# Kernel tuning notes

Hardware: AMD Instinct MI355X
Metric: run time of the kernel (lower is better)

Reference implementation:

```python
import jax, jax.numpy as jnp
import numpy as np

B, C, H, W = 4, 64, 256, 256
HEADS = 4
HID = 128  # dim * ffn_expansion_factor
EPS = 1e-5


def _ln_chan(x, w, b):
    # LayerNorm over channel axis of [b,c,h,w] (equiv to to_3d -> LN over c -> to_4d)
    mu = x.mean(1, keepdims=True)
    var = jnp.mean((x - mu) ** 2, axis=1, keepdims=True)
    return (x - mu) / jnp.sqrt(var + EPS) * w[None, :, None, None] + b[None, :, None, None]


def _ln_last(x, w, b):
    mu = x.mean(-1, keepdims=True)
    var = jnp.mean((x - mu) ** 2, axis=-1, keepdims=True)
    return (x - mu) / jnp.sqrt(var + EPS) * w + b


def _conv1(x, Wt):
    # 1x1 conv, no bias; Wt: [out,in]
    return jnp.einsum('oi,bihw->bohw', Wt, x)


def _l2norm(x):
    # torch F.normalize(dim=-1): x / max(||x||, 1e-12)
    return x / jnp.maximum(jnp.linalg.norm(x, axis=-1, keepdims=True), 1e-12)


def _dct(inp1, inp2, Wq, Wk, Wv, temp):
    # Divide_Cross_Transformer: q from inp2, k/v from inp1; channel-wise attention
    b, c, h, w = inp1.shape
    ch = c // HEADS
    hw = h * w
    q = _conv1(inp2, Wq).reshape(b, HEADS, ch, hw)
    k = _conv1(inp1, Wk).reshape(b, HEADS, ch, hw)
    v = _conv1(inp1, Wv).reshape(b, HEADS, ch, hw)
    q = _l2norm(q)
    k = _l2norm(k)
    attn = jax.nn.softmax(jnp.einsum('bhcn,bhdn->bhcd', q, k) * temp[None], axis=-1)
    return attn, v  # attn: [b,head,ch,ch], v: [b,head,ch,hw]


def _ffn(x3, w1, b1, w2, b2):
    # torch nn.GELU default = exact erf
    hdn = jax.nn.gelu(jnp.einsum('bnc,hc->bnh', x3, w1) + b1, approximate=False)
    return jnp.einsum('bnh,ch->bnc', hdn, w2) + b2


def setup_inputs() -> dict:
    key = jax.random.key(0)
    ks = jax.random.split(key, 16)
    s = 0.05

    def n(k, shape):
        return jax.random.normal(k, shape, jnp.float32) * s

    ones = jnp.ones((C,), jnp.float32)
    zeros = jnp.zeros((C,), jnp.float32)
    return {
        'image': jax.random.normal(ks[0], (B, C, H, W), jnp.float32),
        'event': jax.random.normal(ks[1], (B, C, H, W), jnp.float32),
        'Wq_c': n(ks[2], (C, C)), 'Wk_c': n(ks[3], (C, C)), 'Wv_c': n(ks[4], (C, C)),
        'temp_c': jnp.ones((HEADS, 1, 1), jnp.float32),
        'Wq_d': n(ks[5], (C, C)), 'Wk_d': n(ks[6], (C, C)), 'Wv_d': n(ks[7], (C, C)),
        'temp_d': jnp.ones((HEADS, 1, 1), jnp.float32),
        'ln_img_w': ones, 'ln_img_b': zeros,
        'ln_evt_w': ones, 'ln_evt_b': zeros,
        'ln_com_w': ones, 'ln_com_b': zeros,
        'ln_dif_w': ones, 'ln_dif_b': zeros,
        'ln1_w': ones, 'ln1_b': zeros,
        'ln2_w': ones, 'ln2_b': zeros,
        'fc1c_w': n(ks[8], (HID, C)), 'fc1c_b': jnp.zeros((HID,), jnp.float32),
        'fc2c_w': n(ks[9], (C, HID)), 'fc2c_b': jnp.zeros((C,), jnp.float32),
        'fc1d_w': n(ks[10], (HID, C)), 'fc1d_b': jnp.zeros((HID,), jnp.float32),
        'fc2d_w': n(ks[11], (C, HID)), 'fc2d_b': jnp.zeros((C,), jnp.float32),
        'proj1_w': n(ks[12], (C, C)), 'proj2_w': n(ks[13], (C, C)),
    }


def reference(image, event, Wq_c, Wk_c, Wv_c, temp_c, Wq_d, Wk_d, Wv_d, temp_d,
              ln_img_w, ln_img_b, ln_evt_w, ln_evt_b, ln_com_w, ln_com_b,
              ln_dif_w, ln_dif_b, ln1_w, ln1_b, ln2_w, ln2_b,
              fc1c_w, fc1c_b, fc2c_w, fc2c_b, fc1d_w, fc1d_b, fc2d_w, fc2d_b,
              proj1_w, proj2_w):
    b, c, h, w = image.shape
    hw = h * w
    common = image + event
    differential = image - event

    ni = _ln_chan(image, ln_img_w, ln_img_b)
    ne = _ln_chan(event, ln_evt_w, ln_evt_b)
    nc = _ln_chan(common, ln_com_w, ln_com_b)
    nd = _ln_chan(differential, ln_dif_w, ln_dif_b)

    # common branch: shared conv weights (attn_common), attn maps multiplied
    a_ic, v_ic = _dct(ni, nc, Wq_c, Wk_c, Wv_c, temp_c)
    a_ec, v_ec = _dct(ne, nc, Wq_c, Wk_c, Wv_c, temp_c)
    a_c = a_ic * a_ec
    oc = jnp.einsum('bhcd,bhdn->bhcn', a_c, v_ic + v_ec)  # same attn for both matmuls
    oc = oc.reshape(b, c, h, w)
    oc = _conv1(oc, proj1_w)
    oc3 = oc.reshape(b, c, hw).transpose(0, 2, 1)  # b (hw) c
    oc3 = oc3 + _ffn(_ln_last(oc3, ln1_w, ln1_b), fc1c_w, fc1c_b, fc2c_w, fc2c_b)
    out_common = oc3.transpose(0, 2, 1).reshape(b, c, h, w)

    # differential branch: separate attn maps, not multiplied
    a_id, v_id = _dct(ni, nd, Wq_d, Wk_d, Wv_d, temp_d)
    a_ed, v_ed = _dct(ne, nd, Wq_d, Wk_d, Wv_d, temp_d)
    od = (jnp.einsum('bhcd,bhdn->bhcn', a_id, v_id)
          + jnp.einsum('bhcd,bhdn->bhcn', a_ed, v_ed))
    od = od.reshape(b, c, h, w)
    od = _conv1(od, proj2_w)
    od3 = od.reshape(b, c, hw).transpose(0, 2, 1)
    od3 = od3 + _ffn(_ln_last(od3, ln2_w, ln2_b), fc1d_w, fc1d_b, fc2d_w, fc2d_b)
    out_differential = od3.transpose(0, 2, 1).reshape(b, c, h, w)

    return (out_common, out_differential)
```

## Files before the change

### kernel.cpp

```cpp
#include <hip/hip_runtime.h>
#include <math.h>

typedef unsigned int u32;
typedef unsigned short u16;
typedef __attribute__((ext_vector_type(8))) short short8;
typedef __attribute__((ext_vector_type(4))) float float4v;

#define NBATCH 4
#define HW 65536

#define OFF_COV 0
#define OFF_T   131072
#define OFF_M   294912
#define OFF_P   344064
#define OFF_WC  393216
#define OFF_PAR 516096
#define WS_NEED ((size_t)(OFF_PAR + 1048576) * 4)

__device__ inline float bf2f(u16 h){ return __uint_as_float(((u32)h) << 16); }
__device__ inline u16 f2bf(float x){
  u32 u = __float_as_uint(x);
  u += 0x7fffu + ((u >> 16) & 1u);
  return (u16)(u >> 16);
}
__device__ inline u32 packbf2(float a, float b){
  return (u32)f2bf(a) | ((u32)f2bf(b) << 16);
}
__device__ inline float bfu(u32 u, int hi){
  return __uint_as_float(hi ? (u & 0xffff0000u) : (u << 16));
}

__device__ inline bool detect_f32(const void* probe, int t, int* s_cnt){
  if (t == 0) *s_cnt = 0;
  __syncthreads();
  u32 w = ((const u32*)probe)[t & 255];
  u32 ex = (w >> 7) & 0xffu;
  if (!(ex >= 113u && ex <= 133u)) atomicAdd(s_cnt, 1);
  __syncthreads();
  return *s_cnt >= 128;
}

__device__ inline void ld8(const u16* pb, const float* pf, size_t idx, bool f32, float* o){
  if (f32){
    const float4 a = *(const float4*)(pf + idx);
    const float4 b = *(const float4*)(pf + idx + 4);
    o[0]=a.x; o[1]=a.y; o[2]=a.z; o[3]=a.w; o[4]=b.x; o[5]=b.y; o[6]=b.z; o[7]=b.w;
  } else {
    uint4 r = *(const uint4*)(pb + idx);
    const u32* p = (const u32*)&r;
    #pragma unroll
    for (int j=0;j<8;j++) o[j] = bfu(p[j>>1], j&1);
  }
}

__device__ inline void softmax16(float* l){
  float m = l[0];
  #pragma unroll
  for (int i=1;i<16;i++) m = fmaxf(m, l[i]);
  float s = 0.f;
  #pragma unroll
  for (int i=0;i<16;i++){ l[i] = __expf(l[i]-m); s += l[i]; }
  float r = 1.0f/s;
  #pragma unroll
  for (int i=0;i<16;i++) l[i] *= r;
}

__global__ __launch_bounds__(256) void convert_all(
    const void* img,
    const void* t0, const void* t1, const void* t2, const void* t3,
    const void* t4, const void* t5, const void* t6, const void* t7,
    const void* t8, const void* t9, const void* t10, const void* t11,
    const void* t12, const void* t13, const void* t14, const void* t15,
    const void* t16, const void* t17, const void* t18, const void* t19,
    const void* t20, const void* t21, const void* t22, const void* t23,
    const void* t24, const void* t25, const void* t26, const void* t27,
    const void* t28, const void* t29,
    u16* __restrict__ wc)
{
  __shared__ int s_cnt;
  const int t = threadIdx.x;
  const bool f32 = detect_f32(img, t, &s_cnt);
  const int sizes[30] = {4096,4096,4096,4,4096,4096,4096,4,
                         64,64,64,64,64,64,64,64,64,64,64,64,
                         8192,128,8192,64,8192,128,8192,64,4096,4096};
  const void* srcs[30] = {t0,t1,t2,t3,t4,t5,t6,t7,t8,t9,t10,t11,t12,t13,t14,
                          t15,t16,t17,t18,t19,t20,t21,t22,t23,t24,t25,t26,t27,t28,t29};
  const int id = blockIdx.x;
  const void* s = srcs[id];
  const int n = sizes[id];
  u16* d = wc + (size_t)id*8192;
  for (int j = t; j < n; j += 256)
    d[j] = f32 ? f2bf(((const float*)s)[j]) : ((const u16*)s)[j];
}

__global__ __launch_bounds__(256) void k1_cov(
    const void* __restrict__ img, const void* __restrict__ evt,
    const u16* __restrict__ lniw, const u16* __restrict__ lnib,
    const u16* __restrict__ lnew, const u16* __restrict__ lneb,
    const u16* __restrict__ lncw, const u16* __restrict__ lncb,
    const u16* __restrict__ lndw, const u16* __restrict__ lndb,
    float* __restrict__ cov, float* __restrict__ par, int use_par)
{
  __shared__ u16 NtL[4*64*72];
  __shared__ float spart[4][64][5];
  __shared__ float params[64][8];
  __shared__ int s_cnt;

  const int t = threadIdx.x;
  const bool f32 = detect_f32(img, t, &s_cnt);
  const u16* imgb = (const u16*)img; const float* imgf = (const float*)img;
  const u16* evtb = (const u16*)evt; const float* evtf = (const float*)evt;

  const int b = blockIdx.x >> 7;
  const int P0 = (blockIdx.x & 127) * 512;
  const int chg = t >> 3, pg = t & 7, ch0 = chg*2;
  const int wave = t >> 6, lane = t & 63, l15 = lane & 15, quad = lane >> 4;

  float wi0=bf2f(lniw[ch0]), wi1=bf2f(lniw[ch0+1]);
  float bi0=bf2f(lnib[ch0]), bi1=bf2f(lnib[ch0+1]);
  float we0=bf2f(lnew[ch0]), we1=bf2f(lnew[ch0+1]);
  float be0=bf2f(lneb[ch0]), be1=bf2f(lneb[ch0+1]);
  float wc0=bf2f(lncw[ch0]), wc1=bf2f(lncw[ch0+1]);
  float bc0=bf2f(lncb[ch0]), bc1=bf2f(lncb[ch0+1]);
  float wd0=bf2f(lndw[ch0]), wd1=bf2f(lndw[ch0+1]);
  float bd0=bf2f(lndb[ch0]), bd1=bf2f(lndb[ch0+1]);

  int va1, vb1, va2, vb2;
  if (wave == 0){ va1=2; vb1=2; va2=2; vb2=0; }
  else if (wave == 1){ va1=2; vb1=1; va2=0; vb2=0; }
  else if (wave == 2){ va1=3; vb1=3; va2=3; vb2=0; }
  else { va1=3; vb1=1; va2=1; vb2=1; }

  float4v acc0[4][4], acc1v[4][4];
  #pragma unroll
  for (int i=0;i<4;i++)
    #pragma unroll
    for (int j=0;j<4;j++){ acc0[i][j]=(float4v)0.f; acc1v[i][j]=(float4v)0.f; }

  const size_t base_i = (size_t)(b*64 + ch0) * HW;

  for (int it = 0; it < 8; ++it){
    const int p0 = P0 + it*64;
    float A0[8], A1[8], B0[8], B1[8];
    ld8(imgb, imgf, base_i + p0 + pg*8, f32, A0);
    ld8(imgb, imgf, base_i + HW + p0 + pg*8, f32, A1);
    ld8(evtb, evtf, base_i + p0 + pg*8, f32, B0);
    ld8(evtb, evtf, base_i + HW + p0 + pg*8, f32, B1);

    float si[8], sii[8], se[8], see[8], sie[8];
    #pragma unroll
    for (int j=0;j<8;j++){
      float xi0=A0[j], xi1=A1[j], xe0=B0[j], xe1=B1[j];
      si[j]  = xi0 + xi1;
      sii[j] = fmaf(xi0, xi0, xi1*xi1);
      se[j]  = xe0 + xe1;
      see[j] = fmaf(xe0, xe0, xe1*xe1);
      sie[j] = fmaf(xi0, xe0, xi1*xe1);
    }
    #pragma unroll
    for (int m=8; m<=32; m<<=1){
      #pragma unroll
      for (int j=0;j<8;j++){
        si[j]  += __shfl_xor(si[j],  m);
        sii[j] += __shfl_xor(sii[j], m);
        se[j]  += __shfl_xor(se[j],  m);
        see[j] += __shfl_xor(see[j], m);
        sie[j] += __shfl_xor(sie[j], m);
      }
    }
    if ((chg & 7) == 0){
      #pragma unroll
      for (int j=0;j<8;j++){
        spart[wave][pg*8+j][0]=si[j];  spart[wave][pg*8+j][1]=sii[j];
        spart[wave][pg*8+j][2]=se[j];  spart[wave][pg*8+j][3]=see[j];
        spart[wave][pg*8+j][4]=sie[j];
      }
    }
    __syncthreads();
    if (t < 64){
      float S0=0,S1=0,S2=0,S3=0,S4=0;
      #pragma unroll
      for (int w=0;w<4;w++){
        S0+=spart[w][t][0]; S1+=spart[w][t][1]; S2+=spart[w][t][2];
        S3+=spart[w][t][3]; S4+=spart[w][t][4];
      }
      const float inv = 0.015625f;
      float mu_i=S0*inv, mu_e=S2*inv;
      float r_i = rsqrtf(fmaf(S1,inv,-mu_i*mu_i)+1e-5f);
      float r_e = rsqrtf(fmaf(S3,inv,-mu_e*mu_e)+1e-5f);
      float mu_c=mu_i+mu_e, mu_d=mu_i-mu_e;
      float r_c = rsqrtf((S1+2.f*S4+S3)*inv - mu_c*mu_c + 1e-5f);
      float r_d = rsqrtf((S1-2.f*S4+S3)*inv - mu_d*mu_d + 1e-5f);
      params[t][0]=mu_i; params[t][1]=r_i; params[t][2]=mu_e; params[t][3]=r_e;
      params[t][4]=mu_c; params[t][5]=r_c; params[t][6]=mu_d; params[t][7]=r_d;
      if (use_par){
        float4 pv; pv.x=mu_i; pv.y=r_i; pv.z=mu_e; pv.w=r_e;
        *(float4*)(par + ((size_t)b*HW + p0 + t)*4) = pv;
      }
    }
    __syncthreads();
    u32 un[4][2][4];
    #pragma unroll
    for (int jj=0;jj<4;jj++){
      float4 pA0 = *(const float4*)&params[pg*8+jj*2][0];
      float4 pB0 = *(const float4*)&params[pg*8+jj*2][4];
      float4 pA1 = *(const float4*)&params[pg*8+jj*2+1][0];
      float4 pB1 = *(const float4*)&params[pg*8+jj*2+1][4];
      float xiA0=A0[2*jj], xiA1=A1[2*jj], xeA0=B0[2*jj], xeA1=B1[2*jj];
      float xiB0=A0[2*jj+1], xiB1=A1[2*jj+1], xeB0=B0[2*jj+1], xeB1=B1[2*jj+1];
      un[0][0][jj] = packbf2(fmaf((xiA0-pA0.x)*pA0.y, wi0, bi0), fmaf((xiB0-pA1.x)*pA1.y, wi0, bi0));
      un[0][1][jj] = packbf2(fmaf((xiA1-pA0.x)*pA0.y, wi1, bi1), fmaf((xiB1-pA1.x)*pA1.y, wi1, bi1));
      un[1][0][jj] = packbf2(fmaf((xeA0-pA0.z)*pA0.w, we0, be0), fmaf((xeB0-pA1.z)*pA1.w, we0, be0));
      un[1][1][jj] = packbf2(fmaf((xeA1-pA0.z)*pA0.w, we1, be1), fmaf((xeB1-pA1.z)*pA1.w, we1, be1));
      float xcA0=xiA0+xeA0, xcA1=xiA1+xeA1, xcB0=xiB0+xeB0, xcB1=xiB1+xeB1;
      un[2][0][jj] = packbf2(fmaf((xcA0-pB0.x)*pB0.y, wc0, bc0), fmaf((xcB0-pB1.x)*pB1.y, wc0, bc0));
      un[2][1][jj] = packbf2(fmaf((xcA1-pB0.x)*pB0.y, wc1, bc1), fmaf((xcB1-pB1.x)*pB1.y, wc1, bc1));
      float xdA0=xiA0-xeA0, xdA1=xiA1-xeA1, xdB0=xiB0-xeB0, xdB1=xiB1-xeB1;
      un[3][0][jj] = packbf2(fmaf((xdA0-pB0.z)*pB0.w, wd0, bd0), fmaf((xdB0-pB1.z)*pB1.w, wd0, bd0));
      un[3][1][jj] = packbf2(fmaf((xdA1-pB0.z)*pB0.w, wd1, bd1), fmaf((xdB1-pB1.z)*pB1.w, wd1, bd1));
    }
    #pragma unroll
    for (int v=0; v<4; v++){
      *(uint4*)&NtL[(v*64 + ch0  )*72 + pg*8] = make_uint4(un[v][0][0],un[v][0][1],un[v][0][2],un[v][0][3]);
      *(uint4*)&NtL[(v*64 + ch0+1)*72 + pg*8] = make_uint4(un[v][1][0],un[v][1][1],un[v][1][2],un[v][1][3]);
    }
    __syncthreads();
    #pragma unroll
    for (int ks=0; ks<2; ks++){
      const int off = ks*32 + quad*8;
      short8 A1f[4], B1f[4], A2f[4], B2f[4];
      #pragma unroll
      for (int mi=0;mi<4;mi++){
        A1f[mi] = *(const short8*)&NtL[(va1*64 + mi*16 + l15)*72 + off];
        B1f[mi] = *(const short8*)&NtL[(vb1*64 + mi*16 + l15)*72 + off];
        A2f[mi] = *(const short8*)&NtL[(va2*64 + mi*16 + l15)*72 + off];
        B2f[mi] = *(const short8*)&NtL[(vb2*64 + mi*16 + l15)*72 + off];
      }
      #pragma unroll
      for (int mi=0;mi<4;mi++)
        #pragma unroll
        for (int nj=0;nj<4;nj++){
          acc0[mi][nj]  = __builtin_amdgcn_mfma_f32_16x16x32_bf16(A1f[mi], B1f[nj], acc0[mi][nj], 0,0,0);
          acc1v[mi][nj] = __builtin_amdgcn_mfma_f32_16x16x32_bf16(A2f[mi], B2f[nj], acc1v[mi][nj], 0,0,0);
        }
    }
  }
  float* c0 = cov + ((size_t)(wave*2 + 0)*NBATCH + b)*4096;
  float* c1 = cov + ((size_t)(wave*2 + 1)*NBATCH + b)*4096;
  #pragma unroll
  for (int mi=0;mi<4;mi++)
    #pragma unroll
    for (int nj=0;nj<4;nj++){
      int row0 = mi*16 + quad*4, col = nj*16 + l15;
      #pragma unroll
      for (int r=0;r<4;r++){
        atomicAdd(&c0[(row0+r)*64 + col], acc0[mi][nj][r]);
        atomicAdd(&c1[(row0+r)*64 + col], acc1v[mi][nj][r]);
      }
    }
}

__global__ __launch_bounds__(256) void p2a(
    const u16* __restrict__ Wq_c, const u16* __restrict__ Wk_c,
    const u16* __restrict__ Wq_d, const u16* __restrict__ Wk_d,
    float* __restrict__ ws)
{
  __shared__ float WL[64][65];
  __shared__ float CL[64][64];
  const int t = threadIdx.x;
  const int b = blockIdx.x & 3;
  const int which = blockIdx.x >> 2;
  int wsel, csel;
  switch (which){
    case 0: wsel=0; csel=0; break;
    case 1: wsel=1; csel=3; break;
    case 2: wsel=1; csel=7; break;
    case 3: wsel=2; csel=4; break;
    case 4: wsel=3; csel=3; break;
    case 5: wsel=3; csel=7; break;
    case 6: wsel=0; csel=1; break;
    case 7: wsel=0; csel=2; break;
    case 8: wsel=2; csel=5; break;
    default: wsel=2; csel=6; break;
  }
  const u16* W = (wsel==0)? Wq_c : (wsel==1)? Wk_c : (wsel==2)? Wq_d : Wk_d;
  const float* Cm = ws + ((size_t)csel*NBATCH + b)*4096;
  { int r = t>>2, c0 = (t&3)*16;
    #pragma unroll
    for (int i=0;i<16;i++) WL[r][c0+i] = bf2f(W[r*64 + c0 + i]);
    const float4* s = (const float4*)(Cm + r*64 + c0);
    float4* d = (float4*)&CL[r][c0];
    d[0]=s[0]; d[1]=s[1]; d[2]=s[2]; d[3]=s[3]; }
  __syncthreads();
  const int r = t>>2, k0 = (t&3)*16;
  float a[16];
  #pragma unroll
  for (int i=0;i<16;i++) a[i]=0.f;
  for (int m=0;m<64;m++){
    float wv = WL[r][m];
    #pragma unroll
    for (int i=0;i<16;i++) a[i] = fmaf(wv, CL[m][k0+i], a[i]);
  }
  float* o = ws + OFF_T + ((size_t)which*NBATCH + b)*4096 + r*64 + k0;
  #pragma unroll
  for (int i=0;i<16;i++) o[i] = a[i];
}

__global__ __launch_bounds__(256) void p2b(
    float* __restrict__ ws,
    const u16* __restrict__ Wq_c, const u16* __restrict__ Wk_c,
    const u16* __restrict__ Wq_d, const u16* __restrict__ Wk_d,
    const u16* __restrict__ Wv_c, const u16* __restrict__ Wv_d,
    const u16* __restrict__ temp_c, const u16* __restrict__ temp_d)
{
  const int b = blockIdx.x, t = threadIdx.x;
  __shared__ float rn[6][64];
  __shared__ float GLs[4][64][16];
  __shared__ float AL[3][64][16];
  const float* T = ws + OFF_T;
  {
    int s = t>>6, c = t&63;
    const float* Tp = T + ((size_t)s*NBATCH + b)*4096 + c*64;
    const u16* Wp = (s==0)? Wq_c : (s==3)? Wq_d : Wk_c;
    float acc=0;
    for (int k=0;k<64;k++) acc = fmaf(Tp[k], bf2f(Wp[c*64+k]), acc);
    rn[s][c] = 1.0f/fmaxf(sqrtf(fmaxf(acc,0.f)), 1e-12f);
    if (t < 128){
      int s2 = 4 + (t>>6);
      const float* Tp2 = T + ((size_t)s2*NBATCH + b)*4096 + c*64;
      float acc2=0;
      for (int k=0;k<64;k++) acc2 = fmaf(Tp2[k], bf2f(Wk_d[c*64+k]), acc2);
      rn[s2][c] = 1.0f/fmaxf(sqrtf(fmaxf(acc2,0.f)), 1e-12f);
    }
  }
  #pragma unroll 1
  for (int i=0;i<16;i++){
    int e = t*16 + i;
    int s = e >> 10, c = (e>>4)&63, dl = e&15, d = (c&~15)+dl;
    const float* Tp = T + ((size_t)(6+s)*NBATCH + b)*4096 + c*64;
    const u16* Wp = ((s<2)? Wk_c : Wk_d) + d*64;
    float acc=0;
    for (int j=0;j<64;j++) acc = fmaf(Tp[j], bf2f(Wp[j]), acc);
    GLs[s][c][dl] = acc;
  }
  __syncthreads();
  if (t < 192){
    int set = t>>6, c = t&63, h = c>>4, cb = c&~15;
    if (set == 0){
      float tc = bf2f(temp_c[h]);
      float rq = rn[0][c];
      float l1[16], l2[16];
      #pragma unroll
      for (int dl=0;dl<16;dl++){
        l1[dl] = GLs[0][c][dl]*rq*rn[1][cb+dl]*tc;
        l2[dl] = GLs[1][c][dl]*rq*rn[2][cb+dl]*tc;
      }
      softmax16(l1); softmax16(l2);
      #pragma unroll
      for (int dl=0;dl<16;dl++) AL[0][c][dl] = l1[dl]*l2[dl];
    } else {
      float td = bf2f(temp_d[h]);
      float rq = rn[3][c];
      int gi = (set==1)? 2 : 3;
      int rk = (set==1)? 4 : 5;
      float l[16];
      #pragma unroll
      for (int dl=0;dl<16;dl++) l[dl] = GLs[gi][c][dl]*rq*rn[rk][cb+dl]*td;
      softmax16(l);
      #pragma unroll
      for (int dl=0;dl<16;dl++) AL[set][c][dl] = l[dl];
    }
  }
  __syncthreads();
  for (int wsel=0; wsel<3; wsel++){
    const u16* Wv = (wsel==0)? Wv_c : Wv_d;
    #pragma unroll 1
    for (int i=0;i<16;i++){
      int e = t*16+i, c = e>>6, k = e&63, cb = c&~15;
      float acc=0;
      #pragma unroll
      for (int dl=0;dl<16;dl++) acc = fmaf(AL[wsel][c][dl], bf2f(Wv[(cb+dl)*64 + k]), acc);
      ws[OFF_M + ((size_t)wsel*NBATCH + b)*4096 + c*64 + k] = acc;
    }
  }
}

__global__ __launch_bounds__(256) void p2c(
    const u16* __restrict__ proj1, const u16* __restrict__ proj2,
    float* __restrict__ ws)
{
  __shared__ float WL[64][65];
  __shared__ float CL[64][64];
  const int t = threadIdx.x;
  const int b = blockIdx.x & 3;
  const int which = blockIdx.x >> 2;
  const u16* W = (which==0)? proj1 : proj2;
  const float* Cm = ws + OFF_M + ((size_t)which*NBATCH + b)*4096;
  { int r = t>>2, c0 = (t&3)*16;
    #pragma unroll
    for (int i=0;i<16;i++) WL[r][c0+i] = bf2f(W[r*64 + c0 + i]);
    const float4* s = (const float4*)(Cm + r*64 + c0);
    float4* d = (float4*)&CL[r][c0];
    d[0]=s[0]; d[1]=s[1]; d[2]=s[2]; d[3]=s[3]; }
  __syncthreads();
  const int r = t>>2, k0 = (t&3)*16;
  float a[16];
  #pragma unroll
  for (int i=0;i<16;i++) a[i]=0.f;
  for (int m=0;m<64;m++){
    float wv = WL[r][m];
    #pragma unroll
    for (int i=0;i<16;i++) a[i] = fmaf(wv, CL[m][k0+i], a[i]);
  }
  float* o = ws + OFF_P + ((size_t)which*NBATCH + b)*4096 + r*64 + k0;
  #pragma unroll
  for (int i=0;i<16;i++) o[i] = a[i];
}

__global__ __launch_bounds__(256) void k3_common(
    const void* __restrict__ img, const void* __restrict__ evt,
    const u16* __restrict__ lniw, const u16* __restrict__ lnib,
    const u16* __restrict__ lnew, const u16* __restrict__ lneb,
    const u16* __restrict__ ln1w, const u16* __restrict__ ln1b,
    const u16* __restrict__ fc1w, const u16* __restrict__ fc1b,
    const u16* __restrict__ fc2w, const u16* __restrict__ fc2b,
    const float* __restrict__ Pmat, void* __restrict__ outp, size_t obase,
    const float* __restrict__ par, int use_par)
{
  __shared__ u16 fc1L[128*72];
  __shared__ u16 fc2L[64*136];
  __shared__ u16 PcL[64*72];
  __shared__ u16 SB[64*136];
  __shared__ float spart[4][64][4];
  __shared__ float params[64][4];
  __shared__ float b1L[128];
  __shared__ float b2L[64];
  __shared__ int s_cnt;

  const int t = threadIdx.x;
  const bool f32 = detect_f32(img, t, &s_cnt);
  const u16* imgb = (const u16*)img; const float* imgf = (const float*)img;
  const u16* evtb = (const u16*)evt; const float* evtf = (const float*)evt;

  const int b = blockIdx.x >> 8;
  const int P0 = (blockIdx.x & 255) * 256;
  const int chg = t >> 3, pg = t & 7, ch0 = chg*2;
  const int wave = t >> 6, lane = t & 63, l15 = lane & 15, quad = lane >> 4;

  { int row = t >> 1, c0 = (t & 1)*32;
    const uint4* s = (const uint4*)(fc1w + row*64 + c0);
    uint4* d = (uint4*)&fc1L[row*72 + c0];
    d[0]=s[0]; d[1]=s[1]; d[2]=s[2]; d[3]=s[3]; }
  { int row = t >> 2, c0 = (t & 3)*32;
    const uint4* s = (const uint4*)(fc2w + row*128 + c0);
    uint4* d = (uint4*)&fc2L[row*136 + c0];
    d[0]=s[0]; d[1]=s[1]; d[2]=s[2]; d[3]=s[3]; }
  { int row = t >> 2, c0 = (t & 3)*16;
    const float* s = Pmat + (size_t)b*4096 + row*64 + c0;
    u32 u[8];
    #pragma unroll
    for (int i=0;i<8;i++) u[i] = packbf2(s[2*i], s[2*i+1]);
    uint4* d = (uint4*)&PcL[row*72 + c0];
    d[0] = make_uint4(u[0],u[1],u[2],u[3]);
    d[1] = make_uint4(u[4],u[5],u[6],u[7]); }
  if (t < 128) b1L[t] = bf2f(fc1b[t]);
  if (t < 64)  b2L[t] = bf2f(fc2b[t]);

  float wi0=bf2f(lniw[ch0]), wi1=bf2f(lniw[ch0+1]);
  float we0=bf2f(lnew[ch0]), we1=bf2f(lnew[ch0+1]);
  float bs0=bf2f(lnib[ch0]) + bf2f(lneb[ch0]);
  float bs1=bf2f(lnib[ch0+1]) + bf2f(lneb[ch0+1]);
  float w1r[4], b1r[4];
  #pragma unroll
  for (int nj=0;nj<4;nj++){ w1r[nj]=bf2f(ln1w[nj*16+l15]); b1r[nj]=bf2f(ln1b[nj*16+l15]); }
  __syncthreads();

  const size_t base_i = (size_t)(b*64 + ch0)*HW;
  for (int it=0; it<4; ++it){
    const int p0 = P0 + it*64;
    float A0[8], A1[8], B0[8], B1[8];
    ld8(imgb, imgf, base_i + p0 + pg*8, f32, A0);
    ld8(imgb, imgf, base_i + HW + p0 + pg*8, f32, A1);
    ld8(evtb, evtf, base_i + p0 + pg*8, f32, B0);
    ld8(evtb, evtf, base_i + HW + p0 + pg*8, f32, B1);

    if (use_par){
      const float4* pp = (const float4*)(par + ((size_t)b*HW + p0 + pg*8)*4);
      #pragma unroll
      for (int j=0;j<8;j++){
        float4 pr = pp[j];
        float a0=(A0[j]-pr.x)*pr.y, a1=(A1[j]-pr.x)*pr.y;
        float c0f=(B0[j]-pr.z)*pr.w, c1f=(B1[j]-pr.z)*pr.w;
        float n0 = fmaf(a0, wi0, fmaf(c0f, we0, bs0));
        float n1 = fmaf(a1, wi1, fmaf(c1f, we1, bs1));
        *(u32*)&SB[(pg*8+j)*136 + ch0] = packbf2(n0, n1);
      }
    } else {
      float si[8], sii[8], se[8], see[8];
      #pragma unroll
      for (int j=0;j<8;j++){
        float xi0=A0[j], xi1=A1[j], xe0=B0[j], xe1=B1[j];
        si[j]=xi0+xi1; sii[j]=fmaf(xi0,xi0,xi1*xi1);
        se[j]=xe0+xe1; see[j]=fmaf(xe0,xe0,xe1*xe1);
      }
      #pragma unroll
      for (int m=8;m<=32;m<<=1)
        #pragma unroll
        for (int j=0;j<8;j++){
          si[j]+=__shfl_xor(si[j],m); sii[j]+=__shfl_xor(sii[j],m);
          se[j]+=__shfl_xor(se[j],m); see[j]+=__shfl_xor(see[j],m);
        }
      if ((chg&7)==0){
        #pragma unroll
        for (int j=0;j<8;j++){
          spart[wave][pg*8+j][0]=si[j]; spart[wave][pg*8+j][1]=sii[j];
          spart[wave][pg*8+j][2]=se[j]; spart[wave][pg*8+j][3]=see[j];
        }
      }
      __syncthreads();
      if (t<64){
        float S0=0,S1=0,S2=0,S3=0;
        #pragma unroll
        for (int w=0;w<4;w++){ S0+=spart[w][t][0]; S1+=spart[w][t][1]; S2+=spart[w][t][2]; S3+=spart[w][t][3]; }
        const float inv=0.015625f;
        float mu_i=S0*inv, mu_e=S2*inv;
        float r_i=rsqrtf(fmaf(S1,inv,-mu_i*mu_i)+1e-5f);
        float r_e=rsqrtf(fmaf(S3,inv,-mu_e*mu_e)+1e-5f);
        params[t][0]=mu_i; params[t][1]=r_i; params[t][2]=mu_e; params[t][3]=r_e;
      }
      __syncthreads();
      #pragma unroll
      for (int j=0;j<8;j++){
        float4 pr = *(const float4*)&params[pg*8+j][0];
        float a0=(A0[j]-pr.x)*pr.y, a1=(A1[j]-pr.x)*pr.y;
        float c0f=(B0[j]-pr.z)*pr.w, c1f=(B1[j]-pr.z)*pr.w;
        float n0 = fmaf(a0, wi0, fmaf(c0f, we0, bs0));
        float n1 = fmaf(a1, wi1, fmaf(c1f, we1, bs1));
        *(u32*)&SB[(pg*8+j)*136 + ch0] = packbf2(n0, n1);
      }
    }
    __syncthreads();
    float4v acc1[4];
    #pragma unroll
    for (int nj=0;nj<4;nj++) acc1[nj]=(float4v)0.f;
    const int px_row = wave*16 + l15;
    #pragma unroll
    for (int ks=0;ks<2;ks++){
      const int off = ks*32 + quad*8;
      short8 af = *(const short8*)&SB[px_row*136 + off];
      #pragma unroll
      for (int nj=0;nj<4;nj++){
        short8 bw = *(const short8*)&PcL[(nj*16+l15)*72 + off];
        acc1[nj] = __builtin_amdgcn_mfma_f32_16x16x32_bf16(af, bw, acc1[nj], 0,0,0);
      }
    }
    float s[4], sq[4];
    #pragma unroll
    for (int j=0;j<4;j++){
      s[j] = acc1[0][j]+acc1[1][j]+acc1[2][j]+acc1[3][j];
      sq[j] = acc1[0][j]*acc1[0][j];
      sq[j] = fmaf(acc1[1][j],acc1[1][j],sq[j]);
      sq[j] = fmaf(acc1[2][j],acc1[2][j],sq[j]);
      sq[j] = fmaf(acc1[3][j],acc1[3][j],sq[j]);
    }
    #pragma unroll
    for (int m=1;m<=8;m<<=1)
      #pragma unroll
      for (int j=0;j<4;j++){ s[j]+=__shfl_xor(s[j],m); sq[j]+=__shfl_xor(sq[j],m); }
    float muj[4], rj[4];
    #pragma unroll
    for (int j=0;j<4;j++){
      muj[j]=s[j]*0.015625f;
      rj[j]=rsqrtf(fmaf(sq[j],0.015625f,-muj[j]*muj[j])+1e-5f);
    }
    #pragma unroll
    for (int nj=0;nj<4;nj++)
      #pragma unroll
      for (int j=0;j<4;j++){
        float tv = (acc1[nj][j]-muj[j])*rj[j];
        tv = fmaf(tv, w1r[nj], b1r[nj]);
        SB[(wave*16+quad*4+j)*136 + nj*16+l15] = f2bf(tv);
      }
    float4v accF[8];
    #pragma unroll
    for (int nh=0;nh<8;nh++) accF[nh]=(float4v)0.f;
    #pragma unroll
    for (int ks=0;ks<2;ks++){
      const int off = ks*32+quad*8;
      short8 af = *(const short8*)&SB[px_row*136 + off];
      #pragma unroll
      for (int nh=0;nh<8;nh++){
        short8 bw = *(const short8*)&fc1L[(nh*16+l15)*72 + off];
        accF[nh] = __builtin_amdgcn_mfma_f32_16x16x32_bf16(af, bw, accF[nh], 0,0,0);
      }
    }
    #pragma unroll
    for (int nh=0;nh<8;nh++){
      float bb = b1L[nh*16+l15];
      #pragma unroll
      for (int j=0;j<4;j++){
        float v = accF[nh][j] + bb;
        float g = 0.5f*v*(1.0f + erff(v*0.70710678118654752f));
        SB[(wave*16+quad*4+j)*136 + nh*16+l15] = f2bf(g);
      }
    }
    float4v accO[4];
    #pragma unroll
    for (int nj=0;nj<4;nj++) accO[nj]=(float4v)0.f;
    #pragma unroll
    for (int ks=0;ks<4;ks++){
      const int off = ks*32+quad*8;
      short8 ag = *(const short8*)&SB[px_row*136 + off];
      #pragma unroll
      for (int nj=0;nj<4;nj++){
        short8 bw = *(const short8*)&fc2L[(nj*16+l15)*136 + off];
        accO[nj] = __builtin_amdgcn_mfma_f32_16x16x32_bf16(ag, bw, accO[nj], 0,0,0);
      }
    }
    const int px0 = p0 + wave*16 + quad*4;
    #pragma unroll
    for (int nj=0;nj<4;nj++){
      float bb = b2L[nj*16+l15];
      int r = nj*16+l15;
      float v0 = acc1[nj][0] + accO[nj][0] + bb;
      float v1 = acc1[nj][1] + accO[nj][1] + bb;
      float v2 = acc1[nj][2] + accO[nj][2] + bb;
      float v3 = acc1[nj][3] + accO[nj][3] + bb;
      size_t oi = obase + (size_t)(b*64 + r)*HW + px0;
      if (f32){ float4 fv; fv.x=v0; fv.y=v1; fv.z=v2; fv.w=v3;
        *(float4*)((float*)outp + oi) = fv; }
      else *(uint2*)((u16*)outp + oi) = make_uint2(packbf2(v0,v1), packbf2(v2,v3));
    }
    __syncthreads();
  }
}

__global__ __launch_bounds__(256) void k3_diff(
    const void* __restrict__ img, const void* __restrict__ evt,
    const u16* __restrict__ lniw, const u16* __restrict__ lnib,
    const u16* __restrict__ lnew, const u16* __restrict__ lneb,
    const u16* __restrict__ ln2w, const u16* __restrict__ ln2b,
    const u16* __restrict__ fc1w, const u16* __restrict__ fc1b,
    const u16* __restrict__ fc2w, const u16* __restrict__ fc2b,
    const float* __restrict__ Pmat, void* __restrict__ outp, size_t obase,
    const float* __restrict__ par, int use_par)
{
  __shared__ u16 fc1L[128*72];
  __shared__ u16 fc2L[64*136];
  __shared__ u16 PiL[64*72];
  __shared__ u16 PeL[64*72];
  __shared__ u16 N2L[64*144];
  __shared__ float spart[4][64][4];
  __shared__ float params[64][4];
  __shared__ float b1L[128];
  __shared__ float b2L[64];
  __shared__ int s_cnt;

  const int t = threadIdx.x;
  const bool f32 = detect_f32(img, t, &s_cnt);
  const u16* imgb = (const u16*)img; const float* imgf = (const float*)img;
  const u16* evtb = (const u16*)evt; const float* evtf = (const float*)evt;

  const int b = blockIdx.x >> 8;
  const int P0 = (blockIdx.x & 255) * 256;
  const int chg = t >> 3, pg = t & 7, ch0 = chg*2;
  const int wave = t >> 6, lane = t & 63, l15 = lane & 15, quad = lane >> 4;

  { int row = t >> 1, c0 = (t & 1)*32;
    const uint4* s = (const uint4*)(fc1w + row*64 + c0);
    uint4* d = (uint4*)&fc1L[row*72 + c0];
    d[0]=s[0]; d[1]=s[1]; d[2]=s[2]; d[3]=s[3]; }
  { int row = t >> 2, c0 = (t & 3)*32;
    const uint4* s = (const uint4*)(fc2w + row*128 + c0);
    uint4* d = (uint4*)&fc2L[row*136 + c0];
    d[0]=s[0]; d[1]=s[1]; d[2]=s[2]; d[3]=s[3]; }
  { int row = t >> 2, c0 = (t & 3)*16;
    const float* si_ = Pmat + ((size_t)1*NBATCH + b)*4096 + row*64 + c0;
    const float* se_ = Pmat + ((size_t)2*NBATCH + b)*4096 + row*64 + c0;
    u32 u[8];
    #pragma unroll
    for (int i=0;i<8;i++) u[i] = packbf2(si_[2*i], si_[2*i+1]);
    uint4* d = (uint4*)&PiL[row*72 + c0];
    d[0] = make_uint4(u[0],u[1],u[2],u[3]); d[1] = make_uint4(u[4],u[5],u[6],u[7]);
    #pragma unroll
    for (int i=0;i<8;i++) u[i] = packbf2(se_[2*i], se_[2*i+1]);
    uint4* d2 = (uint4*)&PeL[row*72 + c0];
    d2[0] = make_uint4(u[0],u[1],u[2],u[3]); d2[1] = make_uint4(u[4],u[5],u[6],u[7]); }
  if (t < 128) b1L[t] = bf2f(fc1b[t]);
  if (t < 64)  b2L[t] = bf2f(fc2b[t]);

  float wi0=bf2f(lniw[ch0]), wi1=bf2f(lniw[ch0+1]);
  float bi0=bf2f(lnib[ch0]), bi1=bf2f(lnib[ch0+1]);
  float we0=bf2f(lnew[ch0]), we1=bf2f(lnew[ch0+1]);
  float be0=bf2f(lneb[ch0]), be1=bf2f(lneb[ch0+1]);
  float w1r[4], b1r[4];
  #pragma unroll
  for (int nj=0;nj<4;nj++){ w1r[nj]=bf2f(ln2w[nj*16+l15]); b1r[nj]=bf2f(ln2b[nj*16+l15]); }
  __syncthreads();

  const size_t base_i = (size_t)(b*64 + ch0)*HW;
  for (int it=0; it<4; ++it){
    const int p0 = P0 + it*64;
    float A0[8], A1[8], B0[8], B1[8];
    ld8(imgb, imgf, base_i + p0 + pg*8, f32, A0);
    ld8(imgb, imgf, base_i + HW + p0 + pg*8, f32, A1);
    ld8(evtb, evtf, base_i + p0 + pg*8, f32, B0);
    ld8(evtb, evtf, base_i + HW + p0 + pg*8, f32, B1);

    if (use_par){
      const float4* pp = (const float4*)(par + ((size_t)b*HW + p0 + pg*8)*4);
      #pragma unroll
      for (int j=0;j<8;j++){
        float4 pr = pp[j];
        float a0=(A0[j]-pr.x)*pr.y, a1=(A1[j]-pr.x)*pr.y;
        float c0f=(B0[j]-pr.z)*pr.w, c1f=(B1[j]-pr.z)*pr.w;
        *(u32*)&N2L[(pg*8+j)*144 + ch0]      = packbf2(fmaf(a0,wi0,bi0), fmaf(a1,wi1,bi1));
        *(u32*)&N2L[(pg*8+j)*144 + 72 + ch0] = packbf2(fmaf(c0f,we0,be0), fmaf(c1f,we1,be1));
      }
    } else {
      float si[8], sii[8], se[8], see[8];
      #pragma unroll
      for (int j=0;j<8;j++){
        float xi0=A0[j], xi1=A1[j], xe0=B0[j], xe1=B1[j];
        si[j]=xi0+xi1; sii[j]=fmaf(xi0,xi0,xi1*xi1);
        se[j]=xe0+xe1; see[j]=fmaf(xe0,xe0,xe1*xe1);
      }
      #pragma unroll
      for (int m=8;m<=32;m<<=1)
        #pragma unroll
        for (int j=0;j<8;j++){
          si[j]+=__shfl_xor(si[j],m); sii[j]+=__shfl_xor(sii[j],m);
          se[j]+=__shfl_xor(se[j],m); see[j]+=__shfl_xor(see[j],m);
        }
      if ((chg&7)==0){
        #pragma unroll
        for (int j=0;j<8;j++){
          spart[wave][pg*8+j][0]=si[j]; spart[wave][pg*8+j][1]=sii[j];
          spart[wave][pg*8+j][2]=se[j]; spart[wave][pg*8+j][3]=see[j];
        }
      }
      __syncthreads();
      if (t<64){
        float S0=0,S1=0,S2=0,S3=0;
        #pragma unroll
        for (int w=0;w<4;w++){ S0+=spart[w][t][0]; S1+=spart[w][t][1]; S2+=spart[w][t][2]; S3+=spart[w][t][3]; }
        const float inv=0.015625f;
        float mu_i=S0*inv, mu_e=S2*inv;
        float r_i=rsqrtf(fmaf(S1,inv,-mu_i*mu_i)+1e-5f);
        float r_e=rsqrtf(fmaf(S3,inv,-mu_e*mu_e)+1e-5f);
        params[t][0]=mu_i; params[t][1]=r_i; params[t][2]=mu_e; params[t][3]=r_e;
      }
      __syncthreads();
      #pragma unroll
      for (int j=0;j<8;j++){
        float4 pr = *(const float4*)&params[pg*8+j][0];
        float a0=(A0[j]-pr.x)*pr.y, a1=(A1[j]-pr.x)*pr.y;
        float c0f=(B0[j]-pr.z)*pr.w, c1f=(B1[j]-pr.z)*pr.w;
        *(u32*)&N2L[(pg*8+j)*144 + ch0]      = packbf2(fmaf(a0,wi0,bi0), fmaf(a1,wi1,bi1));
        *(u32*)&N2L[(pg*8+j)*144 + 72 + ch0] = packbf2(fmaf(c0f,we0,be0), fmaf(c1f,we1,be1));
      }
    }
    __syncthreads();
    float4v acc1[4];
    #pragma unroll
    for (int nj=0;nj<4;nj++) acc1[nj]=(float4v)0.f;
    const int px_row = wave*16 + l15;
    #pragma unroll
    for (int ks=0;ks<2;ks++){
      const int off = ks*32 + quad*8;
      short8 ai = *(const short8*)&N2L[px_row*144 + off];
      short8 ae = *(const short8*)&N2L[px_row*144 + 72 + off];
      #pragma unroll
      for (int nj=0;nj<4;nj++){
        short8 bwi = *(const short8*)&PiL[(nj*16+l15)*72 + off];
        acc1[nj] = __builtin_amdgcn_mfma_f32_16x16x32_bf16(ai, bwi, acc1[nj], 0,0,0);
        short8 bwe = *(const short8*)&PeL[(nj*16+l15)*72 + off];
        acc1[nj] = __builtin_amdgcn_mfma_f32_16x16x32_bf16(ae, bwe, acc1[nj], 0,0,0);
      }
    }
    float s[4], sq[4];
    #pragma unroll
    for (int j=0;j<4;j++){
      s[j] = acc1[0][j]+acc1[1][j]+acc1[2][j]+acc1[3][j];
      sq[j] = acc1[0][j]*acc1[0][j];
      sq[j] = fmaf(acc1[1][j],acc1[1][j],sq[j]);
      sq[j] = fmaf(acc1[2][j],acc1[2][j],sq[j]);
      sq[j] = fmaf(acc1[3][j],acc1[3][j],sq[j]);
    }
    #pragma unroll
    for (int m=1;m<=8;m<<=1)
      #pragma unroll
      for (int j=0;j<4;j++){ s[j]+=__shfl_xor(s[j],m); sq[j]+=__shfl_xor(sq[j],m); }
    float muj[4], rj[4];
    #pragma unroll
    for (int j=0;j<4;j++){
      muj[j]=s[j]*0.015625f;
      rj[j]=rsqrtf(fmaf(sq[j],0.015625f,-muj[j]*muj[j])+1e-5f);
    }
    #pragma unroll
    for (int nj=0;nj<4;nj++)
      #pragma unroll
      for (int j=0;j<4;j++){
        float tv = (acc1[nj][j]-muj[j])*rj[j];
        tv = fmaf(tv, w1r[nj], b1r[nj]);
        N2L[(wave*16+quad*4+j)*144 + nj*16+l15] = f2bf(tv);
      }
    float4v accF[8];
    #pragma unroll
    for (int nh=0;nh<8;nh++) accF[nh]=(float4v)0.f;
    #pragma unroll
    for (int ks=0;ks<2;ks++){
      const int off = ks*32+quad*8;
      short8 af = *(const short8*)&N2L[px_row*144 + off];
      #pragma unroll
      for (int nh=0;nh<8;nh++){
        short8 bw = *(const short8*)&fc1L[(nh*16+l15)*72 + off];
        accF[nh] = __builtin_amdgcn_mfma_f32_16x16x32_bf16(af, bw, accF[nh], 0,0,0);
      }
    }
    #pragma unroll
    for (int nh=0;nh<8;nh++){
      float bb = b1L[nh*16+l15];
      #pragma unroll
      for (int j=0;j<4;j++){
        float v = accF[nh][j] + bb;
        float g = 0.5f*v*(1.0f + erff(v*0.70710678118654752f));
        N2L[(wave*16+quad*4+j)*144 + nh*16+l15] = f2bf(g);
      }
    }
    float4v accO[4];
    #pragma unroll
    for (int nj=0;nj<4;nj++) accO[nj]=(float4v)0.f;
    #pragma unroll
    for (int ks=0;ks<4;ks++){
      const int off = ks*32+quad*8;
      short8 ag = *(const short8*)&N2L[px_row*144 + off];
      #pragma unroll
      for (int nj=0;nj<4;nj++){
        short8 bw = *(const short8*)&fc2L[(nj*16+l15)*136 + off];
        accO[nj] = __builtin_amdgcn_mfma_f32_16x16x32_bf16(ag, bw, accO[nj], 0,0,0);
      }
    }
    const int px0 = p0 + wave*16 + quad*4;
    #pragma unroll
    for (int nj=0;nj<4;nj++){
      float bb = b2L[nj*16+l15];
      int r = nj*16+l15;
      float v0 = acc1[nj][0] + accO[nj][0] + bb;
      float v1 = acc1[nj][1] + accO[nj][1] + bb;
      float v2 = acc1[nj][2] + accO[nj][2] + bb;
      float v3 = acc1[nj][3] + accO[nj][3] + bb;
      size_t oi = obase + (size_t)(b*64 + r)*HW + px0;
      if (f32){ float4 fv; fv.x=v0; fv.y=v1; fv.z=v2; fv.w=v3;
        *(float4*)((float*)outp + oi) = fv; }
      else *(uint2*)((u16*)outp + oi) = make_uint2(packbf2(v0,v1), packbf2(v2,v3));
    }
    __syncthreads();
  }
}

extern "C" void kernel_launch(void* const* d_in, const int* in_sizes, int n_in,
                              void* d_out, int out_size, void* d_ws, size_t ws_size,
                              hipStream_t stream)
{
  const void* img = d_in[0];
  const void* evt = d_in[1];
  float* ws = (float*)d_ws;
  u16* wc = (u16*)(ws + OFF_WC);
  float* par = ws + OFF_PAR;
  const int use_par = (ws_size >= WS_NEED) ? 1 : 0;
  #define SLOT(i) (wc + (size_t)((i)-2)*8192)

  hipMemsetAsync(ws, 0, 131072*sizeof(float), stream);
  convert_all<<<dim3(30), dim3(256), 0, stream>>>(img,
      d_in[2], d_in[3], d_in[4], d_in[5], d_in[6], d_in[7], d_in[8], d_in[9],
      d_in[10], d_in[11], d_in[12], d_in[13], d_in[14], d_in[15], d_in[16], d_in[17],
      d_in[18], d_in[19], d_in[20], d_in[21], d_in[22], d_in[23], d_in[24], d_in[25],
      d_in[26], d_in[27], d_in[28], d_in[29], d_in[30], d_in[31], wc);
  k1_cov<<<dim3(512), dim3(256), 0, stream>>>(img, evt,
      SLOT(10), SLOT(11), SLOT(12), SLOT(13), SLOT(14), SLOT(15), SLOT(16), SLOT(17),
      ws, par, use_par);
  p2a<<<dim3(40), dim3(256), 0, stream>>>(SLOT(2), SLOT(3), SLOT(6), SLOT(7), ws);
  p2b<<<dim3(4), dim3(256), 0, stream>>>(ws, SLOT(2), SLOT(3), SLOT(6), SLOT(7),
      SLOT(4), SLOT(8), SLOT(5), SLOT(9));
  p2c<<<dim3(12), dim3(256), 0, stream>>>(SLOT(30), SLOT(31), ws);
  k3_common<<<dim3(1024), dim3(256), 0, stream>>>(img, evt,
      SLOT(10), SLOT(11), SLOT(12), SLOT(13), SLOT(18), SLOT(19),
      SLOT(22), SLOT(23), SLOT(24), SLOT(25), ws + OFF_P, d_out, (size_t)0, par, use_par);
  k3_diff<<<dim3(1024), dim3(256), 0, stream>>>(img, evt,
      SLOT(10), SLOT(11), SLOT(12), SLOT(13), SLOT(20), SLOT(21),
      SLOT(26), SLOT(27), SLOT(28), SLOT(29), ws + OFF_P, d_out, (size_t)16777216, par, use_par);
  #undef SLOT
}
```

Measured before the change: 629.6 us.

## Double k1_cov threads to 512, one channel and one covariance product per wave

```diff
diff --git a/kernel.cpp b/kernel.cpp
--- a/kernel.cpp
+++ b/kernel.cpp
@@ -24,7 +24,9 @@
   return (u16)(u >> 16);
 }
 __device__ inline u32 packbf2(float a, float b){
-  return (u32)f2bf(a) | ((u32)f2bf(b) << 16);
+  u32 r;
+  asm("v_cvt_pk_bf16_f32 %0, %1, %2" : "=v"(r) : "v"(a), "v"(b));
+  return r;
 }
 __device__ inline float bfu(u32 u, int hi){
   return __uint_as_float(hi ? (u & 0xffff0000u) : (u << 16));
@@ -36,6 +38,18 @@
   u32 w = ((const u32*)probe)[t & 255];
   u32 ex = (w >> 7) & 0xffu;
   if (!(ex >= 113u && ex <= 133u)) atomicAdd(s_cnt, 1);
+  __syncthreads();
+  return *s_cnt >= 128;
+}
+
+__device__ inline bool detect_f32_512(const void* probe, int t, int* s_cnt){
+  if (t == 0) *s_cnt = 0;
+  __syncthreads();
+  if (t < 256){
+    u32 w = ((const u32*)probe)[t];
+    u32 ex = (w >> 7) & 0xffu;
+    if (!(ex >= 113u && ex <= 133u)) atomicAdd(s_cnt, 1);
+  }
   __syncthreads();
   return *s_cnt >= 128;
 }
@@ -93,7 +107,7 @@
     d[j] = f32 ? f2bf(((const float*)s)[j]) : ((const u16*)s)[j];
 }
 
-__global__ __launch_bounds__(256) void k1_cov(
+__global__ __launch_bounds__(512, 4) void k1_cov(
     const void* __restrict__ img, const void* __restrict__ evt,
     const u16* __restrict__ lniw, const u16* __restrict__ lnib,
     const u16* __restrict__ lnew, const u16* __restrict__ lneb,
@@ -102,85 +116,72 @@
     float* __restrict__ cov, float* __restrict__ par, int use_par)
 {
   __shared__ u16 NtL[4*64*72];
-  __shared__ float spart[4][64][5];
-  __shared__ float params[64][8];
+  __shared__ float spart[8][64][5];
+  __shared__ float params[8][64];
   __shared__ int s_cnt;
 
   const int t = threadIdx.x;
-  const bool f32 = detect_f32(img, t, &s_cnt);
+  const bool f32 = detect_f32_512(img, t, &s_cnt);
   const u16* imgb = (const u16*)img; const float* imgf = (const float*)img;
   const u16* evtb = (const u16*)evt; const float* evtf = (const float*)evt;
 
   const int b = blockIdx.x >> 7;
   const int P0 = (blockIdx.x & 127) * 512;
-  const int chg = t >> 3, pg = t & 7, ch0 = chg*2;
+  const int ch = t >> 3, pg = t & 7;
   const int wave = t >> 6, lane = t & 63, l15 = lane & 15, quad = lane >> 4;
 
-  float wi0=bf2f(lniw[ch0]), wi1=bf2f(lniw[ch0+1]);
-  float bi0=bf2f(lnib[ch0]), bi1=bf2f(lnib[ch0+1]);
-  float we0=bf2f(lnew[ch0]), we1=bf2f(lnew[ch0+1]);
-  float be0=bf2f(lneb[ch0]), be1=bf2f(lneb[ch0+1]);
-  float wc0=bf2f(lncw[ch0]), wc1=bf2f(lncw[ch0+1]);
-  float bc0=bf2f(lncb[ch0]), bc1=bf2f(lncb[ch0+1]);
-  float wd0=bf2f(lndw[ch0]), wd1=bf2f(lndw[ch0+1]);
-  float bd0=bf2f(lndb[ch0]), bd1=bf2f(lndb[ch0+1]);
-
-  int va1, vb1, va2, vb2;
-  if (wave == 0){ va1=2; vb1=2; va2=2; vb2=0; }
-  else if (wave == 1){ va1=2; vb1=1; va2=0; vb2=0; }
-  else if (wave == 2){ va1=3; vb1=3; va2=3; vb2=0; }
-  else { va1=3; vb1=1; va2=1; vb2=1; }
-
-  float4v acc0[4][4], acc1v[4][4];
+  float wi=bf2f(lniw[ch]), bi=bf2f(lnib[ch]);
+  float we=bf2f(lnew[ch]), be=bf2f(lneb[ch]);
+  float wc_=bf2f(lncw[ch]), bc_=bf2f(lncb[ch]);
+  float wd_=bf2f(lndw[ch]), bd_=bf2f(lndb[ch]);
+
+  const int va = (wave==3)?0 : (wave==7)?1 : (wave<3)?2:3;
+  const int vb = (wave==0)?2 : (wave==4)?3 :
+                 ((wave==2)||(wave==6)||(wave==7))?1:0;
+
+  float4v acc[4][4];
   #pragma unroll
   for (int i=0;i<4;i++)
     #pragma unroll
-    for (int j=0;j<4;j++){ acc0[i][j]=(float4v)0.f; acc1v[i][j]=(float4v)0.f; }
-
-  const size_t base_i = (size_t)(b*64 + ch0) * HW;
+    for (int j=0;j<4;j++) acc[i][j]=(float4v)0.f;
+
+  const size_t base = (size_t)(b*64 + ch) * HW;
 
   for (int it = 0; it < 8; ++it){
     const int p0 = P0 + it*64;
-    float A0[8], A1[8], B0[8], B1[8];
-    ld8(imgb, imgf, base_i + p0 + pg*8, f32, A0);
-    ld8(imgb, imgf, base_i + HW + p0 + pg*8, f32, A1);
-    ld8(evtb, evtf, base_i + p0 + pg*8, f32, B0);
-    ld8(evtb, evtf, base_i + HW + p0 + pg*8, f32, B1);
-
-    float si[8], sii[8], se[8], see[8], sie[8];
-    #pragma unroll
-    for (int j=0;j<8;j++){
-      float xi0=A0[j], xi1=A1[j], xe0=B0[j], xe1=B1[j];
-      si[j]  = xi0 + xi1;
-      sii[j] = fmaf(xi0, xi0, xi1*xi1);
-      se[j]  = xe0 + xe1;
-      see[j] = fmaf(xe0, xe0, xe1*xe1);
-      sie[j] = fmaf(xi0, xe0, xi1*xe1);
-    }
-    #pragma unroll
-    for (int m=8; m<=32; m<<=1){
-      #pragma unroll
-      for (int j=0;j<8;j++){
-        si[j]  += __shfl_xor(si[j],  m);
-        sii[j] += __shfl_xor(sii[j], m);
-        se[j]  += __shfl_xor(se[j],  m);
-        see[j] += __shfl_xor(see[j], m);
-        sie[j] += __shfl_xor(sie[j], m);
-      }
-    }
-    if ((chg & 7) == 0){
-      #pragma unroll
-      for (int j=0;j<8;j++){
-        spart[wave][pg*8+j][0]=si[j];  spart[wave][pg*8+j][1]=sii[j];
-        spart[wave][pg*8+j][2]=se[j];  spart[wave][pg*8+j][3]=see[j];
-        spart[wave][pg*8+j][4]=sie[j];
+    float A[8], B[8];
+    ld8(imgb, imgf, base + p0 + pg*8, f32, A);
+    ld8(evtb, evtf, base + p0 + pg*8, f32, B);
+
+    #pragma unroll 1
+    for (int jp=0;jp<4;jp++){
+      float xa=A[2*jp], xb=A[2*jp+1], ea=B[2*jp], eb=B[2*jp+1];
+      float s0a=xa,     s0b=xb;
+      float s1a=xa*xa,  s1b=xb*xb;
+      float s2a=ea,     s2b=eb;
+      float s3a=ea*ea,  s3b=eb*eb;
+      float s4a=xa*ea,  s4b=xb*eb;
+      #pragma unroll
+      for (int m=8;m<=32;m<<=1){
+        s0a+=__shfl_xor(s0a,m); s0b+=__shfl_xor(s0b,m);
+        s1a+=__shfl_xor(s1a,m); s1b+=__shfl_xor(s1b,m);
+        s2a+=__shfl_xor(s2a,m); s2b+=__shfl_xor(s2b,m);
+        s3a+=__shfl_xor(s3a,m); s3b+=__shfl_xor(s3b,m);
+        s4a+=__shfl_xor(s4a,m); s4b+=__shfl_xor(s4b,m);
+      }
+      if ((ch&7)==0){
+        int px = pg*8 + 2*jp;
+        spart[wave][px][0]=s0a; spart[wave][px][1]=s1a; spart[wave][px][2]=s2a;
+        spart[wave][px][3]=s3a; spart[wave][px][4]=s4a;
+        spart[wave][px+1][0]=s0b; spart[wave][px+1][1]=s1b; spart[wave][px+1][2]=s2b;
+        spart[wave][px+1][3]=s3b; spart[wave][px+1][4]=s4b;
       }
     }
     __syncthreads();
     if (t < 64){
       float S0=0,S1=0,S2=0,S3=0,S4=0;
       #pragma unroll
-      for (int w=0;w<4;w++){
+      for (int w=0;w<8;w++){
         S0+=spart[w][t][0]; S1+=spart[w][t][1]; S2+=spart[w][t][2];
         S3+=spart[w][t][3]; S4+=spart[w][t][4];
       }
@@ -191,72 +192,75 @@
       float mu_c=mu_i+mu_e, mu_d=mu_i-mu_e;
       float r_c = rsqrtf((S1+2.f*S4+S3)*inv - mu_c*mu_c + 1e-5f);
       float r_d = rsqrtf((S1-2.f*S4+S3)*inv - mu_d*mu_d + 1e-5f);
-      params[t][0]=mu_i; params[t][1]=r_i; params[t][2]=mu_e; params[t][3]=r_e;
-      params[t][4]=mu_c; params[t][5]=r_c; params[t][6]=mu_d; params[t][7]=r_d;
+      params[0][t]=mu_i; params[1][t]=r_i; params[2][t]=mu_e; params[3][t]=r_e;
+      params[4][t]=mu_c; params[5][t]=r_c; params[6][t]=mu_d; params[7][t]=r_d;
       if (use_par){
         float4 pv; pv.x=mu_i; pv.y=r_i; pv.z=mu_e; pv.w=r_e;
         *(float4*)(par + ((size_t)b*HW + p0 + t)*4) = pv;
       }
     }
     __syncthreads();
-    u32 un[4][2][4];
-    #pragma unroll
-    for (int jj=0;jj<4;jj++){
-      float4 pA0 = *(const float4*)&params[pg*8+jj*2][0];
-      float4 pB0 = *(const float4*)&params[pg*8+jj*2][4];
-      float4 pA1 = *(const float4*)&params[pg*8+jj*2+1][0];
-      float4 pB1 = *(const float4*)&params[pg*8+jj*2+1][4];
-      float xiA0=A0[2*jj], xiA1=A1[2*jj], xeA0=B0[2*jj], xeA1=B1[2*jj];
-      float xiB0=A0[2*jj+1], xiB1=A1[2*jj+1], xeB0=B0[2*jj+1], xeB1=B1[2*jj+1];
-      un[0][0][jj] = packbf2(fmaf((xiA0-pA0.x)*pA0.y, wi0, bi0), fmaf((xiB0-pA1.x)*pA1.y, wi0, bi0));
-      un[0][1][jj] = packbf2(fmaf((xiA1-pA0.x)*pA0.y, wi1, bi1), fmaf((xiB1-pA1.x)*pA1.y, wi1, bi1));
-      un[1][0][jj] = packbf2(fmaf((xeA0-pA0.z)*pA0.w, we0, be0), fmaf((xeB0-pA1.z)*pA1.w, we0, be0));
-      un[1][1][jj] = packbf2(fmaf((xeA1-pA0.z)*pA0.w, we1, be1), fmaf((xeB1-pA1.z)*pA1.w, we1, be1));
-      float xcA0=xiA0+xeA0, xcA1=xiA1+xeA1, xcB0=xiB0+xeB0, xcB1=xiB1+xeB1;
-      un[2][0][jj] = packbf2(fmaf((xcA0-pB0.x)*pB0.y, wc0, bc0), fmaf((xcB0-pB1.x)*pB1.y, wc0, bc0));
-      un[2][1][jj] = packbf2(fmaf((xcA1-pB0.x)*pB0.y, wc1, bc1), fmaf((xcB1-pB1.x)*pB1.y, wc1, bc1));
-      float xdA0=xiA0-xeA0, xdA1=xiA1-xeA1, xdB0=xiB0-xeB0, xdB1=xiB1-xeB1;
-      un[3][0][jj] = packbf2(fmaf((xdA0-pB0.z)*pB0.w, wd0, bd0), fmaf((xdB0-pB1.z)*pB1.w, wd0, bd0));
-      un[3][1][jj] = packbf2(fmaf((xdA1-pB0.z)*pB0.w, wd1, bd1), fmaf((xdB1-pB1.z)*pB1.w, wd1, bd1));
-    }
-    #pragma unroll
-    for (int v=0; v<4; v++){
-      *(uint4*)&NtL[(v*64 + ch0  )*72 + pg*8] = make_uint4(un[v][0][0],un[v][0][1],un[v][0][2],un[v][0][3]);
-      *(uint4*)&NtL[(v*64 + ch0+1)*72 + pg*8] = make_uint4(un[v][1][0],un[v][1][1],un[v][1][2],un[v][1][3]);
+
+    {
+      u32 u0[4], u1[4];
+      #pragma unroll
+      for (int jj=0;jj<4;jj++){
+        int px = pg*8 + 2*jj;
+        float2 mi01 = *(const float2*)&params[0][px];
+        float2 ri01 = *(const float2*)&params[1][px];
+        float2 me01 = *(const float2*)&params[2][px];
+        float2 re01 = *(const float2*)&params[3][px];
+        u0[jj] = packbf2(fmaf((A[2*jj]-mi01.x)*ri01.x, wi, bi),
+                         fmaf((A[2*jj+1]-mi01.y)*ri01.y, wi, bi));
+        u1[jj] = packbf2(fmaf((B[2*jj]-me01.x)*re01.x, we, be),
+                         fmaf((B[2*jj+1]-me01.y)*re01.y, we, be));
+      }
+      *(uint4*)&NtL[(0*64+ch)*72 + pg*8] = make_uint4(u0[0],u0[1],u0[2],u0[3]);
+      *(uint4*)&NtL[(1*64+ch)*72 + pg*8] = make_uint4(u1[0],u1[1],u1[2],u1[3]);
+      #pragma unroll
+      for (int jj=0;jj<4;jj++){
+        int px = pg*8 + 2*jj;
+        float2 mc01 = *(const float2*)&params[4][px];
+        float2 rc01 = *(const float2*)&params[5][px];
+        float2 md01 = *(const float2*)&params[6][px];
+        float2 rd01 = *(const float2*)&params[7][px];
+        float xc0=A[2*jj]+B[2*jj], xc1=A[2*jj+1]+B[2*jj+1];
+        float xd0=A[2*jj]-B[2*jj], xd1=A[2*jj+1]-B[2*jj+1];
+        u0[jj] = packbf2(fmaf((xc0-mc01.x)*rc01.x, wc_, bc_),
+                         fmaf((xc1-mc01.y)*rc01.y, wc_, bc_));
+        u1[jj] = packbf2(fmaf((xd0-md01.x)*rd01.x, wd_, bd_),
+                         fmaf((xd1-md01.y)*rd01.y, wd_, bd_));
+      }
+      *(uint4*)&NtL[(2*64+ch)*72 + pg*8] = make_uint4(u0[0],u0[1],u0[2],u0[3]);
+      *(uint4*)&NtL[(3*64+ch)*72 + pg*8] = make_uint4(u1[0],u1[1],u1[2],u1[3]);
     }
     __syncthreads();
+
     #pragma unroll
     for (int ks=0; ks<2; ks++){
       const int off = ks*32 + quad*8;
-      short8 A1f[4], B1f[4], A2f[4], B2f[4];
+      short8 Af[4], Bf[4];
       #pragma unroll
       for (int mi=0;mi<4;mi++){
-        A1f[mi] = *(const short8*)&NtL[(va1*64 + mi*16 + l15)*72 + off];
-        B1f[mi] = *(const short8*)&NtL[(vb1*64 + mi*16 + l15)*72 + off];
-        A2f[mi] = *(const short8*)&NtL[(va2*64 + mi*16 + l15)*72 + off];
-        B2f[mi] = *(const short8*)&NtL[(vb2*64 + mi*16 + l15)*72 + off];
+        Af[mi] = *(const short8*)&NtL[(va*64 + mi*16 + l15)*72 + off];
+        Bf[mi] = *(const short8*)&NtL[(vb*64 + mi*16 + l15)*72 + off];
       }
       #pragma unroll
       for (int mi=0;mi<4;mi++)
         #pragma unroll
-        for (int nj=0;nj<4;nj++){
-          acc0[mi][nj]  = __builtin_amdgcn_mfma_f32_16x16x32_bf16(A1f[mi], B1f[nj], acc0[mi][nj], 0,0,0);
-          acc1v[mi][nj] = __builtin_amdgcn_mfma_f32_16x16x32_bf16(A2f[mi], B2f[nj], acc1v[mi][nj], 0,0,0);
-        }
-    }
-  }
-  float* c0 = cov + ((size_t)(wave*2 + 0)*NBATCH + b)*4096;
-  float* c1 = cov + ((size_t)(wave*2 + 1)*NBATCH + b)*4096;
+        for (int nj=0;nj<4;nj++)
+          acc[mi][nj] = __builtin_amdgcn_mfma_f32_16x16x32_bf16(Af[mi], Bf[nj], acc[mi][nj], 0,0,0);
+    }
+  }
+  float* cg = cov + ((size_t)wave*NBATCH + b)*4096;
   #pragma unroll
   for (int mi=0;mi<4;mi++)
     #pragma unroll
     for (int nj=0;nj<4;nj++){
       int row0 = mi*16 + quad*4, col = nj*16 + l15;
       #pragma unroll
-      for (int r=0;r<4;r++){
-        atomicAdd(&c0[(row0+r)*64 + col], acc0[mi][nj][r]);
-        atomicAdd(&c1[(row0+r)*64 + col], acc1v[mi][nj][r]);
-      }
+      for (int r=0;r<4;r++)
+        atomicAdd(&cg[(row0+r)*64 + col], acc[mi][nj][r]);
     }
 }
 
@@ -877,7 +881,7 @@
       d_in[10], d_in[11], d_in[12], d_in[13], d_in[14], d_in[15], d_in[16], d_in[17],
       d_in[18], d_in[19], d_in[20], d_in[21], d_in[22], d_in[23], d_in[24], d_in[25],
       d_in[26], d_in[27], d_in[28], d_in[29], d_in[30], d_in[31], wc);
-  k1_cov<<<dim3(512), dim3(256), 0, stream>>>(img, evt,
+  k1_cov<<<dim3(512), dim3(512), 0, stream>>>(img, evt,
       SLOT(10), SLOT(11), SLOT(12), SLOT(13), SLOT(14), SLOT(15), SLOT(16), SLOT(17),
       ws, par, use_par);
   p2a<<<dim3(40), dim3(256), 0, stream>>>(SLOT(2), SLOT(3), SLOT(6), SLOT(7), ws);
```

Result: faster. 567.9 us (-9.8%).
